# Kernel tuning notes

Hardware: AMD Instinct MI355X
Metric: run time of the kernel (lower is better)

The kernel has to match this reference:

```python
import jax, jax.numpy as jnp
import numpy as np

B, T, D, P, NP = 32, 512, 512, 200, 8
RADIUS = 3
TEMP = 1.0
DIRECTION = 'right'
NEG = -100000.0
EPS_NORM = 1e-12


def setup_inputs() -> dict:
    key = jax.random.key(0)
    k1, k2, k3 = jax.random.split(key, 3)
    return {
        "x": jax.random.normal(k1, (B, T, D), dtype=jnp.float32),
        "timeline_mask": jnp.ones((B, T), dtype=jnp.float32),
        "prototype_vectors": jax.random.uniform(k2, (P, D, NP), dtype=jnp.float32),
        "patch_select": jax.random.normal(k3, (1, P, NP), dtype=jnp.float32),
    }


def _l2norm(v, axis):
    return v / jnp.maximum(jnp.linalg.norm(v, axis=axis, keepdims=True), EPS_NORM)


def reference(x, timeline_mask, prototype_vectors, patch_select):
    # --- subpatch_dist ---
    xn = _l2norm(x, axis=-1)                       # (B, T, D)
    pn = _l2norm(prototype_vectors, axis=1)        # (P, D, n_p)
    dist_all = jnp.einsum('btd,pdi->bpti', xn, pn)  # (B, P, T, n_p)

    # timeline mask
    tm = timeline_mask[:, None, :, None]
    dist_all = dist_all * tm + (1.0 - tm) * NEG

    dt = dist_all.dtype
    b, p, t, n_p = dist_all.shape
    ar_t = jnp.arange(t)

    mask_act = jnp.ones((b, p, t), dt)
    mask_subpatch = jnp.ones((b, p, n_p), dt)
    mask_all = jnp.ones((b, p, t, n_p), dt)
    adjacent = jnp.ones((b, p, t), dt)

    ids_list, vals_list, ev_list = [], [], []
    # greedy iterative max-select over the n_p subpatches (sequential dependency)
    for it in range(n_p):
        dm = dist_all + (1.0 - mask_all * adjacent[..., None]) * NEG
        max_subs = dm.max(axis=2)                   # (B, P, n_p) best score per subpatch
        max_subs_id = jnp.argmax(dm, axis=2)        # (B, P, n_p) best event per subpatch
        max_sub_act = max_subs.max(axis=-1)         # (B, P)
        sub_id = jnp.argmax(max_subs, axis=-1)      # (B, P) chosen subpatch
        event_id = jnp.take_along_axis(max_subs_id, sub_id[..., None], axis=2)[..., 0]  # (B, P)

        neigh = (jnp.abs(ar_t[None, None, :] - event_id[..., None]) <= RADIUS).astype(dt)
        if it > 0:
            if DIRECTION == 'right':
                dmask = (ar_t[None, None, :] > event_id[..., None]).astype(dt)
            else:
                dmask = (ar_t[None, None, :] < event_id[..., None]).astype(dt)
            neigh = neigh * dmask
        adjacent = neigh

        # suppress chosen event and chosen subpatch (scatter_ 0 == multiply by 1-onehot)
        mask_act = mask_act * (1.0 - jax.nn.one_hot(event_id, t, dtype=dt))
        mask_subpatch = mask_subpatch * (1.0 - jax.nn.one_hot(sub_id, n_p, dtype=dt))
        mask_all = mask_all * mask_act[..., None] * mask_subpatch[:, :, None, :]

        ids_list.append(sub_id)
        vals_list.append(max_sub_act)
        ev_list.append(event_id.astype(dt))

    subpatch_ids = jnp.stack(ids_list, axis=-1)   # (B, P, n_p) int
    values = jnp.stack(vals_list, axis=-1)        # (B, P, n_p)
    indices = jnp.stack(ev_list, axis=-1)         # (B, P, n_p) float, matches torch cat promotion

    order = jnp.argsort(subpatch_ids, axis=-1)    # unique ids -> deterministic permutation
    values_r = jnp.take_along_axis(values, order, axis=-1)
    indices_r = jnp.take_along_axis(indices, order, axis=-1)

    slots = jax.nn.sigmoid(patch_select * TEMP)           # (1, P, n_p)
    factor = slots.sum(-1, keepdims=True) + 1e-10
    values_slot = values_r * (slots * n_p / factor)
    max_activation_slots = values_slot.sum(-1)            # (B, P)
    min_distances = n_p - max_activation_slots
    return (max_activation_slots, min_distances, indices_r)
```

## Files before the change

kernel.cpp:

```cpp
#include <hip/hip_runtime.h>
#include <hip/hip_bf16.h>
#include <hip/hip_fp16.h>
#include <math.h>

#define B_    32
#define T_    512
#define D_    512
#define P_    200
#define NP_   8
#define N_TOT 1600
#define NEG_  (-100000.0f)
#define LO_SCALE 2048.0f
#define LO_INV   (1.0f/2048.0f)

typedef __attribute__((ext_vector_type(8))) _Float16 f16x8;
typedef __attribute__((ext_vector_type(4))) _Float16 f16x4;
typedef __attribute__((ext_vector_type(4))) float   f32x4;

#define GLL16(gp, lp) __builtin_amdgcn_global_load_lds( \
    (const __attribute__((address_space(1))) void*)(gp), \
    (__attribute__((address_space(3))) void*)(lp), 16, 0, 0)

__device__ __forceinline__ float wave_reduce_sum(float v) {
#pragma unroll
  for (int off = 32; off; off >>= 1) v += __shfl_xor(v, off, 64);
  return v;
}

__global__ __launch_bounds__(256) void norm_x_kernel(const float* __restrict__ x,
                                                     _Float16* __restrict__ xh,
                                                     _Float16* __restrict__ xl) {
  int row  = blockIdx.x * 4 + (threadIdx.x >> 6);
  int lane = threadIdx.x & 63;
  const float* xr = x + (size_t)row * D_;
  float4 v0 = *(const float4*)(xr + lane * 4);
  float4 v1 = *(const float4*)(xr + 256 + lane * 4);
  float s = v0.x*v0.x + v0.y*v0.y + v0.z*v0.z + v0.w*v0.w
          + v1.x*v1.x + v1.y*v1.y + v1.z*v1.z + v1.w*v1.w;
  s = wave_reduce_sum(s);
  float dn = fmaxf(sqrtf(s), 1e-12f);
  float f[8] = {v0.x/dn, v0.y/dn, v0.z/dn, v0.w/dn, v1.x/dn, v1.y/dn, v1.z/dn, v1.w/dn};
  f16x4 h0, h1, l0, l1;
#pragma unroll
  for (int j = 0; j < 4; j++) {
    h0[j] = (_Float16)f[j];
    l0[j] = (_Float16)((f[j] - (float)h0[j]) * LO_SCALE);
    h1[j] = (_Float16)f[4 + j];
    l1[j] = (_Float16)((f[4 + j] - (float)h1[j]) * LO_SCALE);
  }
  size_t base = (size_t)row * D_;
  *(f16x4*)(xh + base + lane * 4)       = h0;
  *(f16x4*)(xh + base + 256 + lane * 4) = h1;
  *(f16x4*)(xl + base + lane * 4)       = l0;
  *(f16x4*)(xl + base + 256 + lane * 4) = l1;
}

__global__ __launch_bounds__(256) void norm_w_kernel(const float* __restrict__ proto,
                                                     _Float16* __restrict__ wh,
                                                     _Float16* __restrict__ wl) {
  int n    = blockIdx.x * 4 + (threadIdx.x >> 6);
  int lane = threadIdx.x & 63;
  int p = n >> 3, i = n & 7;
  float v[8];
  float s = 0.f;
#pragma unroll
  for (int k = 0; k < 8; k++) {
    int d = k * 64 + lane;
    v[k] = proto[((size_t)p * D_ + d) * NP_ + i];
    s += v[k] * v[k];
  }
  s = wave_reduce_sum(s);
  float dn = fmaxf(sqrtf(s), 1e-12f);
  size_t base = (size_t)n * D_;
#pragma unroll
  for (int k = 0; k < 8; k++) {
    float f = v[k] / dn;
    _Float16 h = (_Float16)f;
    wh[base + k * 64 + lane] = h;
    wl[base + k * 64 + lane] = (_Float16)((f - (float)h) * LO_SCALE);
  }
}

__global__ __launch_bounds__(256, 2) void gemm_mfma(
    const _Float16* __restrict__ XH, const _Float16* __restrict__ XL,
    const _Float16* __restrict__ WH, const _Float16* __restrict__ WL,
    const float* __restrict__ tm, float* __restrict__ dist) {
  __shared__ _Float16 lds[4 * 128 * 32];
  const int b = blockIdx.z;
  const int n0 = blockIdx.y * 128;
  const int t0 = blockIdx.x * 128;
  const int tid = threadIdx.x;
  const int w = tid >> 6, l = tid & 63;

  int c0 = (w * 2 + 0) * 64 + l;
  int c1 = (w * 2 + 1) * 64 + l;
  int r0 = c0 >> 2, kc0 = (c0 & 3) * 8;
  int r1 = c1 >> 2, kc1 = (c1 & 3) * 8;
  int an0 = n0 + r0; if (an0 > N_TOT - 1) an0 = N_TOT - 1;
  int an1 = n0 + r1; if (an1 > N_TOT - 1) an1 = N_TOT - 1;
  const _Float16* wh0 = WH + (size_t)an0 * D_ + kc0;
  const _Float16* wh1 = WH + (size_t)an1 * D_ + kc1;
  const _Float16* wl0 = WL + (size_t)an0 * D_ + kc0;
  const _Float16* wl1 = WL + (size_t)an1 * D_ + kc1;
  const _Float16* xh0 = XH + ((size_t)b * T_ + t0 + r0) * D_ + kc0;
  const _Float16* xh1 = XH + ((size_t)b * T_ + t0 + r1) * D_ + kc1;
  const _Float16* xl0 = XL + ((size_t)b * T_ + t0 + r0) * D_ + kc0;
  const _Float16* xl1 = XL + ((size_t)b * T_ + t0 + r1) * D_ + kc1;
  _Float16* ldAh = lds +     0 + (w * 2) * 512;
  _Float16* ldAl = lds +  4096 + (w * 2) * 512;
  _Float16* ldXh = lds +  8192 + (w * 2) * 512;
  _Float16* ldXl = lds + 12288 + (w * 2) * 512;

  const int wn = (w >> 1) * 64, wtf = (w & 1) * 64;
  const int fr = l & 15, fq = l >> 4;

  f32x4 acch[4][4], accc[4][4];
#pragma unroll
  for (int m = 0; m < 4; m++)
#pragma unroll
    for (int n = 0; n < 4; n++) { acch[m][n] = (f32x4)0.0f; accc[m][n] = (f32x4)0.0f; }

  for (int k0 = 0; k0 < D_; k0 += 32) {
    GLL16(wh0 + k0, ldAh);
    GLL16(wh1 + k0, ldAh + 512);
    GLL16(wl0 + k0, ldAl);
    GLL16(wl1 + k0, ldAl + 512);
    GLL16(xh0 + k0, ldXh);
    GLL16(xh1 + k0, ldXh + 512);
    GLL16(xl0 + k0, ldXl);
    GLL16(xl1 + k0, ldXl + 512);
    __syncthreads();
    f16x8 ah[4], al[4], bh[4], bl[4];
#pragma unroll
    for (int m = 0; m < 4; m++) {
      int ro = (wn + m * 16 + fr) * 32 + fq * 8;
      ah[m] = *(const f16x8*)&lds[ro];
      al[m] = *(const f16x8*)&lds[4096 + ro];
    }
#pragma unroll
    for (int n = 0; n < 4; n++) {
      int ro = (wtf + n * 16 + fr) * 32 + fq * 8;
      bh[n] = *(const f16x8*)&lds[8192 + ro];
      bl[n] = *(const f16x8*)&lds[12288 + ro];
    }
#pragma unroll
    for (int m = 0; m < 4; m++)
#pragma unroll
      for (int n = 0; n < 4; n++) {
        acch[m][n] = __builtin_amdgcn_mfma_f32_16x16x32_f16(ah[m], bh[n], acch[m][n], 0, 0, 0);
        accc[m][n] = __builtin_amdgcn_mfma_f32_16x16x32_f16(ah[m], bl[n], accc[m][n], 0, 0, 0);
        accc[m][n] = __builtin_amdgcn_mfma_f32_16x16x32_f16(al[m], bh[n], accc[m][n], 0, 0, 0);
      }
    __syncthreads();
  }

#pragma unroll
  for (int n = 0; n < 4; n++) {
    int col = t0 + wtf + n * 16 + fr;
    float tmc = tm[b * T_ + col];
#pragma unroll
    for (int m = 0; m < 4; m++) {
      int nb = n0 + wn + m * 16 + fq * 4;
#pragma unroll
      for (int r = 0; r < 4; r++) {
        int nr = nb + r;
        if (nr < N_TOT) {
          float v = acch[m][n][r] + accc[m][n][r] * LO_INV;
          v = v * tmc + (1.0f - tmc) * NEG_;
          dist[((size_t)b * N_TOT + nr) * T_ + col] = v;
        }
      }
    }
  }
}

__global__ __launch_bounds__(256) void select_kernel(const float* __restrict__ dist,
                                                     const float* __restrict__ tmg,
                                                     const float* __restrict__ psel,
                                                     float* __restrict__ out) {
  __shared__ float sd[4][NP_][T_];
  int w = threadIdx.x >> 6, lane = threadIdx.x & 63;
  int pair = blockIdx.x * 4 + w;
  int b = pair / P_, p = pair % P_;
  const float* dbase = dist + ((size_t)b * N_TOT + p * NP_) * T_;
#pragma unroll
  for (int i = 0; i < NP_; i++) {
    *(float4*)&sd[w][i][lane * 4]       = *(const float4*)(dbase + (size_t)i * T_ + lane * 4);
    *(float4*)&sd[w][i][256 + lane * 4] = *(const float4*)(dbase + (size_t)i * T_ + 256 + lane * 4);
  }
  bool okt = true;
#pragma unroll
  for (int c = 0; c < 8; c++) okt = okt && (tmg[b * T_ + c * 64 + lane] == 1.0f);
  bool tmones = (__ballot(okt) == ~0ULL);
  __syncthreads();

  float valh[8]; int evh[8], sidh[8];
#pragma unroll
  for (int k = 0; k < 8; k++) { valh[k] = 0.f; evh[k] = -1; sidh[k] = 0; }
  unsigned msub = 0xFFu;
  int e_last = 0;

  for (int it = 0; it < 8; ++it) {
    float bv = 0.f; int bkey = 0;
    bool done = false;
    if (tmones && it > 0) {
      int i = lane >> 3, widx = lane & 7;
      int tw, nw;
      if (it == 1) { tw = e_last - 3 + widx; nw = 7; }
      else         { tw = e_last + 1 + widx; nw = 3; }
      bool valid = (widx < nw) && (tw >= 0) && (tw < T_) && (((msub >> i) & 1u) != 0u);
#pragma unroll
      for (int k = 0; k < 8; k++) if (tw == evh[k]) valid = false;
      float v  = valid ? sd[w][i][tw] : -3.0e38f;
      int  key = valid ? (i * T_ + tw) : 0x7FFFFFFF;
#pragma unroll
      for (int off = 32; off; off >>= 1) {
        float ov = __shfl_xor(v, off, 64);
        int  ok2 = __shfl_xor(key, off, 64);
        if (ov > v || (ov == v && ok2 < key)) { v = ov; key = ok2; }
      }
      if (v > -2.9e38f) { bv = v; bkey = key; done = true; }
    }
    if (!done) {
      float lv = -3.0e38f; int lkey = 0x7FFFFFFF;
      for (int i = 0; i < 8; i++) {
        bool sub_ok = ((msub >> i) & 1u) != 0u;
#pragma unroll
        for (int c = 0; c < 8; c++) {
          int t = c * 64 + lane;
          bool act = sub_ok;
          if (it > 0) {
            int dt = t - e_last;
            act = act && (dt <= 3) && (dt >= -3);
            if (it > 1) act = act && (dt > 0);
          }
#pragma unroll
          for (int k = 0; k < 8; k++) if (t == evh[k]) act = false;
          float dv = sd[w][i][t];
          float dm = act ? dv : (dv + NEG_);
          if (dm > lv) { lv = dm; lkey = i * T_ + t; }
        }
      }
#pragma unroll
      for (int off = 32; off; off >>= 1) {
        float ov = __shfl_xor(lv, off, 64);
        int  ok2 = __shfl_xor(lkey, off, 64);
        if (ov > lv || (ov == lv && ok2 < lkey)) { lv = ov; lkey = ok2; }
      }
      bv = lv; bkey = lkey;
    }
    int bi = bkey >> 9, bt = bkey & (T_ - 1);
#pragma unroll
    for (int k = 0; k < 8; k++) {
      if (it == k) { valh[k] = bv; evh[k] = bt; sidh[k] = bi; }
    }
    msub &= ~(1u << bi);
    e_last = bt;
  }

  if (lane == 0) {
    int ord[8]; unsigned used = 0;
#pragma unroll
    for (int j = 0; j < 8; j++) {
      int bk = 1 << 30, bi2 = 0;
#pragma unroll
      for (int k = 0; k < 8; k++)
        if (!((used >> k) & 1u)) { int key = sidh[k] * 8 + k; if (key < bk) { bk = key; bi2 = k; } }
      ord[j] = bi2; used |= 1u << bi2;
    }
    float slots[8]; float ssum = 0.f;
#pragma unroll
    for (int i = 0; i < 8; i++) {
      slots[i] = 1.0f / (1.0f + expf(-psel[p * NP_ + i]));
      ssum += slots[i];
    }
    float fac = ssum + 1e-10f;
    float acc = 0.f;
    float vr[8]; float er[8];
#pragma unroll
    for (int j = 0; j < 8; j++) {
      float vv = 0.f, ee = 0.f;
#pragma unroll
      for (int k = 0; k < 8; k++) if (ord[j] == k) { vv = valh[k]; ee = (float)evh[k]; }
      vr[j] = vv; er[j] = ee;
    }
#pragma unroll
    for (int j = 0; j < 8; j++) acc += vr[j] * (slots[j] * 8.0f / fac);
    int bp = b * P_ + p;
    out[bp] = acc;
    out[B_ * P_ + bp] = 8.0f - acc;
#pragma unroll
    for (int j = 0; j < 8; j++) out[2 * B_ * P_ + bp * 8 + j] = er[j];
  }
}

extern "C" void kernel_launch(void* const* d_in, const int* in_sizes, int n_in,
                              void* d_out, int out_size, void* d_ws, size_t ws_size,
                              hipStream_t stream) {
  const float* x     = (const float*)d_in[0];
  const float* tm    = (const float*)d_in[1];
  const float* proto = (const float*)d_in[2];
  const float* psel  = (const float*)d_in[3];
  float* out = (float*)d_out;

  char* wsb = (char*)d_ws;
  _Float16* XH = (_Float16*)wsb;
  _Float16* XL = (_Float16*)(wsb + 16777216u);
  _Float16* WH = (_Float16*)(wsb + 2u * 16777216u);
  _Float16* WL = (_Float16*)(wsb + 2u * 16777216u + 1638400u);
  float*   dist = (float*)(wsb + 2u * 16777216u + 2u * 1638400u);

  norm_x_kernel<<<dim3(B_ * T_ / 4), 256, 0, stream>>>(x, XH, XL);
  norm_w_kernel<<<dim3(N_TOT / 4), 256, 0, stream>>>(proto, WH, WL);
  gemm_mfma<<<dim3(T_ / 128, (N_TOT + 127) / 128, B_), 256, 0, stream>>>(XH, XL, WH, WL, tm, dist);
  select_kernel<<<dim3(B_ * P_ / 4), 256, 0, stream>>>(dist, tm, psel, out);
}
```

Baseline: 252.1 us.

## Double-buffer GEMM LDS staging and drop LDS copy in select kernel

The GEMM kernel now double-buffers its LDS tiles, prefetching the next K slice while MFMAs run on the current one, and lays each tile out so every lane reads contiguous fragments. The select kernel no longer stages the 8x512 distance rows in shared memory. It computes the first-iteration argmax and the all-masked fallback in one register pass, and reads the small neighbourhood windows straight from global memory. This aims to hide load latency in the GEMM and to cut LDS traffic and footprint in selection. The cost is twice the GEMM LDS use, which may reduce occupancy, plus scattered global reads in the select loop.

```diff
diff --git a/kernel.cpp b/kernel.cpp
--- a/kernel.cpp
+++ b/kernel.cpp
@@ -85,34 +85,50 @@
     const _Float16* __restrict__ XH, const _Float16* __restrict__ XL,
     const _Float16* __restrict__ WH, const _Float16* __restrict__ WL,
     const float* __restrict__ tm, float* __restrict__ dist) {
-  __shared__ _Float16 lds[4 * 128 * 32];
-  const int b = blockIdx.z;
+  __shared__ _Float16 lds[2 * 16384];
+  const int b  = blockIdx.z;
   const int n0 = blockIdx.y * 128;
   const int t0 = blockIdx.x * 128;
   const int tid = threadIdx.x;
   const int w = tid >> 6, l = tid & 63;
-
-  int c0 = (w * 2 + 0) * 64 + l;
-  int c1 = (w * 2 + 1) * 64 + l;
-  int r0 = c0 >> 2, kc0 = (c0 & 3) * 8;
-  int r1 = c1 >> 2, kc1 = (c1 & 3) * 8;
-  int an0 = n0 + r0; if (an0 > N_TOT - 1) an0 = N_TOT - 1;
-  int an1 = n0 + r1; if (an1 > N_TOT - 1) an1 = N_TOT - 1;
-  const _Float16* wh0 = WH + (size_t)an0 * D_ + kc0;
-  const _Float16* wh1 = WH + (size_t)an1 * D_ + kc1;
-  const _Float16* wl0 = WL + (size_t)an0 * D_ + kc0;
-  const _Float16* wl1 = WL + (size_t)an1 * D_ + kc1;
-  const _Float16* xh0 = XH + ((size_t)b * T_ + t0 + r0) * D_ + kc0;
-  const _Float16* xh1 = XH + ((size_t)b * T_ + t0 + r1) * D_ + kc1;
-  const _Float16* xl0 = XL + ((size_t)b * T_ + t0 + r0) * D_ + kc0;
-  const _Float16* xl1 = XL + ((size_t)b * T_ + t0 + r1) * D_ + kc1;
-  _Float16* ldAh = lds +     0 + (w * 2) * 512;
-  _Float16* ldAl = lds +  4096 + (w * 2) * 512;
-  _Float16* ldXh = lds +  8192 + (w * 2) * 512;
-  _Float16* ldXl = lds + 12288 + (w * 2) * 512;
-
-  const int wn = (w >> 1) * 64, wtf = (w & 1) * 64;
-  const int fr = l & 15, fq = l >> 4;
+  const int fr = l & 15;
+  const int lk = (l >> 4) * 8;
+
+  const _Float16* pHi[4]; const _Float16* pLo[4];
+  int dstoff;
+  {
+    int H = w >> 1;
+    if ((w & 1) == 0) {
+#pragma unroll
+      for (int m = 0; m < 4; m++) {
+        int row = n0 + H * 64 + m * 16 + fr;
+        if (row > N_TOT - 1) row = N_TOT - 1;
+        pHi[m] = WH + (size_t)row * D_ + lk;
+        pLo[m] = WL + (size_t)row * D_ + lk;
+      }
+      dstoff = H * 2048;
+    } else {
+#pragma unroll
+      for (int m = 0; m < 4; m++) {
+        int col = t0 + H * 64 + m * 16 + fr;
+        pHi[m] = XH + ((size_t)b * T_ + col) * D_ + lk;
+        pLo[m] = XL + ((size_t)b * T_ + col) * D_ + lk;
+      }
+      dstoff = 8192 + H * 2048;
+    }
+  }
+
+#define STAGE(bufoff, kk) do { \
+    _Float16* dh = &lds[(bufoff) + dstoff]; \
+    _Float16* dl = dh + 4096; \
+    GLL16(pHi[0] + (kk), dh);        GLL16(pHi[1] + (kk), dh + 512); \
+    GLL16(pHi[2] + (kk), dh + 1024); GLL16(pHi[3] + (kk), dh + 1536); \
+    GLL16(pLo[0] + (kk), dl);        GLL16(pLo[1] + (kk), dl + 512); \
+    GLL16(pLo[2] + (kk), dl + 1024); GLL16(pLo[3] + (kk), dl + 1536); \
+  } while (0)
+
+  const int aB = (w >> 1) * 2048;
+  const int xB = 8192 + (w & 1) * 2048;
 
   f32x4 acch[4][4], accc[4][4];
 #pragma unroll
@@ -120,28 +136,23 @@
 #pragma unroll
     for (int n = 0; n < 4; n++) { acch[m][n] = (f32x4)0.0f; accc[m][n] = (f32x4)0.0f; }
 
-  for (int k0 = 0; k0 < D_; k0 += 32) {
-    GLL16(wh0 + k0, ldAh);
-    GLL16(wh1 + k0, ldAh + 512);
-    GLL16(wl0 + k0, ldAl);
-    GLL16(wl1 + k0, ldAl + 512);
-    GLL16(xh0 + k0, ldXh);
-    GLL16(xh1 + k0, ldXh + 512);
-    GLL16(xl0 + k0, ldXl);
-    GLL16(xl1 + k0, ldXl + 512);
-    __syncthreads();
+  STAGE(0, 0);
+  __syncthreads();
+
+  for (int kt = 0; kt < 16; ++kt) {
+    const int cur = (kt & 1) * 16384;
+    if (kt < 15) STAGE(cur ^ 16384, (kt + 1) * 32);
+
     f16x8 ah[4], al[4], bh[4], bl[4];
 #pragma unroll
     for (int m = 0; m < 4; m++) {
-      int ro = (wn + m * 16 + fr) * 32 + fq * 8;
-      ah[m] = *(const f16x8*)&lds[ro];
-      al[m] = *(const f16x8*)&lds[4096 + ro];
+      ah[m] = *(const f16x8*)&lds[cur + aB + m * 512 + l * 8];
+      al[m] = *(const f16x8*)&lds[cur + aB + 4096 + m * 512 + l * 8];
     }
 #pragma unroll
     for (int n = 0; n < 4; n++) {
-      int ro = (wtf + n * 16 + fr) * 32 + fq * 8;
-      bh[n] = *(const f16x8*)&lds[8192 + ro];
-      bl[n] = *(const f16x8*)&lds[12288 + ro];
+      bh[n] = *(const f16x8*)&lds[cur + xB + n * 512 + l * 8];
+      bl[n] = *(const f16x8*)&lds[cur + xB + 4096 + n * 512 + l * 8];
     }
 #pragma unroll
     for (int m = 0; m < 4; m++)
@@ -154,13 +165,14 @@
     __syncthreads();
   }
 
+  const int fq = l >> 4;
 #pragma unroll
   for (int n = 0; n < 4; n++) {
-    int col = t0 + wtf + n * 16 + fr;
+    int col = t0 + (w & 1) * 64 + n * 16 + fr;
     float tmc = tm[b * T_ + col];
 #pragma unroll
     for (int m = 0; m < 4; m++) {
-      int nb = n0 + wn + m * 16 + fq * 4;
+      int nb = n0 + (w >> 1) * 64 + m * 16 + fq * 4;
 #pragma unroll
       for (int r = 0; r < 4; r++) {
         int nr = nb + r;
@@ -172,27 +184,47 @@
       }
     }
   }
+#undef STAGE
 }
 
 __global__ __launch_bounds__(256) void select_kernel(const float* __restrict__ dist,
                                                      const float* __restrict__ tmg,
                                                      const float* __restrict__ psel,
                                                      float* __restrict__ out) {
-  __shared__ float sd[4][NP_][T_];
   int w = threadIdx.x >> 6, lane = threadIdx.x & 63;
   int pair = blockIdx.x * 4 + w;
   int b = pair / P_, p = pair % P_;
   const float* dbase = dist + ((size_t)b * N_TOT + p * NP_) * T_;
-#pragma unroll
-  for (int i = 0; i < NP_; i++) {
-    *(float4*)&sd[w][i][lane * 4]       = *(const float4*)(dbase + (size_t)i * T_ + lane * 4);
-    *(float4*)&sd[w][i][256 + lane * 4] = *(const float4*)(dbase + (size_t)i * T_ + 256 + lane * 4);
-  }
+
   bool okt = true;
 #pragma unroll
   for (int c = 0; c < 8; c++) okt = okt && (tmg[b * T_ + c * 64 + lane] == 1.0f);
   bool tmones = (__ballot(okt) == ~0ULL);
-  __syncthreads();
+
+  float rv = -3.0e38f; int rkey = 0x7FFFFFFF;
+  float qv = -3.0e38f; int qkey = 0x7FFFFFFF;
+#pragma unroll
+  for (int i = 0; i < 8; i++) {
+    const float* row = dbase + (size_t)i * T_;
+    float4 u0 = *(const float4*)(row + lane * 8);
+    float4 u1 = *(const float4*)(row + lane * 8 + 4);
+    float uv[8] = {u0.x, u0.y, u0.z, u0.w, u1.x, u1.y, u1.z, u1.w};
+#pragma unroll
+    for (int j = 0; j < 8; j++) {
+      int key = i * T_ + lane * 8 + j;
+      float v = uv[j];
+      if (v > rv) { rv = v; rkey = key; }
+      float q = v + NEG_;
+      if (q > qv) { qv = q; qkey = key; }
+    }
+  }
+#pragma unroll
+  for (int off = 32; off; off >>= 1) {
+    float ov = __shfl_xor(rv, off, 64); int okk = __shfl_xor(rkey, off, 64);
+    if (ov > rv || (ov == rv && okk < rkey)) { rv = ov; rkey = okk; }
+    float o2 = __shfl_xor(qv, off, 64); int ok2 = __shfl_xor(qkey, off, 64);
+    if (o2 > qv || (o2 == qv && ok2 < qkey)) { qv = o2; qkey = ok2; }
+  }
 
   float valh[8]; int evh[8], sidh[8];
 #pragma unroll
@@ -201,33 +233,39 @@
   int e_last = 0;
 
   for (int it = 0; it < 8; ++it) {
-    float bv = 0.f; int bkey = 0;
-    bool done = false;
-    if (tmones && it > 0) {
-      int i = lane >> 3, widx = lane & 7;
-      int tw, nw;
-      if (it == 1) { tw = e_last - 3 + widx; nw = 7; }
-      else         { tw = e_last + 1 + widx; nw = 3; }
-      bool valid = (widx < nw) && (tw >= 0) && (tw < T_) && (((msub >> i) & 1u) != 0u);
-#pragma unroll
-      for (int k = 0; k < 8; k++) if (tw == evh[k]) valid = false;
-      float v  = valid ? sd[w][i][tw] : -3.0e38f;
-      int  key = valid ? (i * T_ + tw) : 0x7FFFFFFF;
-#pragma unroll
-      for (int off = 32; off; off >>= 1) {
-        float ov = __shfl_xor(v, off, 64);
-        int  ok2 = __shfl_xor(key, off, 64);
-        if (ov > v || (ov == v && ok2 < key)) { v = ov; key = ok2; }
-      }
-      if (v > -2.9e38f) { bv = v; bkey = key; done = true; }
-    }
-    if (!done) {
+    float bv; int bkey;
+    if (tmones) {
+      if (it == 0) { bv = rv; bkey = rkey; }
+      else {
+        int i = lane >> 3, widx = lane & 7;
+        int tw, nw;
+        if (it == 1) { tw = e_last - 3 + widx; nw = 7; }
+        else         { tw = e_last + 1 + widx; nw = 3; }
+        bool valid = (widx < nw) && (tw >= 0) && (tw < T_) && (((msub >> i) & 1u) != 0u);
+#pragma unroll
+        for (int k = 0; k < 8; k++) if (tw == evh[k]) valid = false;
+        float v  = valid ? dbase[(size_t)i * T_ + tw] : -3.0e38f;
+        int  key = valid ? (i * T_ + tw) : 0x7FFFFFFF;
+#pragma unroll
+        for (int off = 32; off; off >>= 1) {
+          float ov = __shfl_xor(v, off, 64);
+          int  ok2 = __shfl_xor(key, off, 64);
+          if (ov > v || (ov == v && ok2 < key)) { v = ov; key = ok2; }
+        }
+        if (v > -2.9e38f) { bv = v; bkey = key; }
+        else              { bv = qv; bkey = qkey; }
+      }
+    } else {
       float lv = -3.0e38f; int lkey = 0x7FFFFFFF;
       for (int i = 0; i < 8; i++) {
         bool sub_ok = ((msub >> i) & 1u) != 0u;
-#pragma unroll
-        for (int c = 0; c < 8; c++) {
-          int t = c * 64 + lane;
+        const float* row = dbase + (size_t)i * T_;
+        float4 u0 = *(const float4*)(row + lane * 8);
+        float4 u1 = *(const float4*)(row + lane * 8 + 4);
+        float uv[8] = {u0.x, u0.y, u0.z, u0.w, u1.x, u1.y, u1.z, u1.w};
+#pragma unroll
+        for (int j = 0; j < 8; j++) {
+          int t = lane * 8 + j;
           bool act = sub_ok;
           if (it > 0) {
             int dt = t - e_last;
@@ -236,8 +274,7 @@
           }
 #pragma unroll
           for (int k = 0; k < 8; k++) if (t == evh[k]) act = false;
-          float dv = sd[w][i][t];
-          float dm = act ? dv : (dv + NEG_);
+          float dm = act ? uv[j] : (uv[j] + NEG_);
           if (dm > lv) { lv = dm; lkey = i * T_ + t; }
         }
       }
```

Result: slower. 260.2 us (+3.2%).
